# Optimization experiments

Hardware: AMD Instinct MI355X
Metric: run time of the kernel (lower is better)

## Reference

```python
import jax, jax.numpy as jnp
import numpy as np

# Perfect 8-ary tree, 6 levels, level-order node indexing.
K = 8            # children per internal node
D = 512          # embedding_dim
P = 8            # number of dependency types (num_params)
OFF = [0, 1, 9, 73, 585, 4681, 37449]  # level start offsets; N = 37449
N = OFF[-1]


def setup_inputs() -> dict:
    key = jax.random.key(0)
    ks = jax.random.split(key, 8)
    s = 1.0 / np.sqrt(D)  # torch default-ish init scale, avoids LSTM saturation
    return {
        "embeddings": jax.random.normal(ks[0], (N, D), dtype=jnp.float32),
        "dep_types": jax.random.randint(ks[1], (N,), 0, P, dtype=jnp.int32),
        "W_dep": jax.random.normal(ks[2], (P, D, D), dtype=jnp.float32) * s,
        "b_dep": jax.random.normal(ks[3], (P, D), dtype=jnp.float32) * s,
        "W_ih": jax.random.normal(ks[4], (4 * D, D), dtype=jnp.float32) * s,
        "W_hh": jax.random.normal(ks[5], (4 * D, D), dtype=jnp.float32) * s,
        "b_ih": jax.random.normal(ks[6], (4 * D,), dtype=jnp.float32) * s,
        "b_hh": jax.random.normal(ks[7], (4 * D,), dtype=jnp.float32) * s,
    }


def _lstm_final_c(seq, W_ih, W_hh, b_ih, b_hh):
    # seq: [B, T, D]; 1-layer LSTM with zero init state; returns final cell state c_T [B, D]
    B = seq.shape[0]
    h0 = jnp.zeros((B, D), seq.dtype)

    def step(carry, z_t):
        h, c = carry
        gates = z_t @ W_ih.T + h @ W_hh.T + b_ih + b_hh  # [B, 4D]
        i, f, g, o = jnp.split(gates, 4, axis=-1)        # torch gate order i,f,g,o
        i, f, o = jax.nn.sigmoid(i), jax.nn.sigmoid(f), jax.nn.sigmoid(o)
        g = jnp.tanh(g)
        c = f * c + i * g
        h = o * jnp.tanh(c)
        return (h, c), None

    (h, c), _ = jax.lax.scan(step, (h0, h0), jnp.swapaxes(seq, 0, 1))
    return c


def reference(embeddings, dep_types, W_dep, b_dep, W_ih, W_hh, b_ih, b_hh):
    # Leaves (level 5): LSTM over length-1 sequence [x] -> final cell state.
    leaf_x = embeddings[OFF[5]:OFF[6]]                       # [32768, D]
    z = _lstm_final_c(leaf_x[:, None, :], W_ih, W_hh, b_ih, b_hh)

    # Level-synchronous bottom-up sweep (exactly the recursion's per-node math).
    for l in range(4, -1, -1):
        m = OFF[l + 1] - OFF[l]                              # nodes at this level
        child_z = z.reshape(m, K, D)                         # children's subtree codes
        child_dep = dep_types[OFF[l + 1]:OFF[l + 2]].reshape(m, K)
        onehot = jax.nn.one_hot(child_dep, P, dtype=child_z.dtype)  # [m, K, P]
        # per-dep Linear: z_c = W_dep[dep] @ x_c + b_dep[dep]
        zc = jnp.einsum('mkj,pij,mkp->mki', child_z, W_dep, onehot) + onehot @ b_dep
        x = embeddings[OFF[l]:OFF[l + 1]]                    # node's own embedding, last in seq
        seq = jnp.concatenate([zc, x[:, None, :]], axis=1)   # [m, K+1, D]
        z = _lstm_final_c(seq, W_ih, W_hh, b_ih, b_hh)

    return z  # root sentence embedding, [1, D]
```

## Files before the change

### kernel.cpp

```cpp
#include <hip/hip_runtime.h>

typedef __attribute__((ext_vector_type(8))) short short8;
typedef __attribute__((ext_vector_type(4))) float f32x4;
typedef _Float16 half_t;

__device__ __forceinline__ unsigned short f2bf(float x){
  union { float f; unsigned u; } v; v.f = x;
  unsigned r = v.u + 0x7fffu + ((v.u >> 16) & 1u);
  return (unsigned short)(r >> 16);
}
__device__ __forceinline__ float sigm(float x){ return 1.0f / (1.0f + __expf(-x)); }
__device__ __forceinline__ float tanh_(float x){
  float e = __expf(2.0f * x);
  return 1.0f - 2.0f / (e + 1.0f);
}
__device__ __forceinline__ short8 load_bf8_f32(const float* p){
  float4 a = *(const float4*)p;
  float4 b = *(const float4*)(p + 4);
  short8 r;
  r[0]=(short)f2bf(a.x); r[1]=(short)f2bf(a.y); r[2]=(short)f2bf(a.z); r[3]=(short)f2bf(a.w);
  r[4]=(short)f2bf(b.x); r[5]=(short)f2bf(b.y); r[6]=(short)f2bf(b.z); r[7]=(short)f2bf(b.w);
  return r;
}
__device__ __forceinline__ f32x4 mfma16(short8 a, short8 b, f32x4 c){
  return __builtin_amdgcn_mfma_f32_16x16x32_bf16(a, b, c, 0, 0, 0);
}
__device__ __forceinline__ void gload16(const void* g, void* lds){
  __builtin_amdgcn_global_load_lds((const __attribute__((address_space(1))) void*)g,
                                   (__attribute__((address_space(3))) void*)lds, 16, 0, 0);
}
__device__ __forceinline__ f32x4 shfl_xor4(f32x4 v, int m){
  f32x4 r;
  r[0]=__shfl_xor(v[0],m); r[1]=__shfl_xor(v[1],m);
  r[2]=__shfl_xor(v[2],m); r[3]=__shfl_xor(v[3],m);
  return r;
}
__device__ __forceinline__ float pick4(f32x4 v, int k){
  float a = (k&1)? v[1] : v[0];
  float b = (k&1)? v[3] : v[2];
  return (k&2)? b : a;
}
__device__ __forceinline__ f32x4 sel4(f32x4 a0, f32x4 a1, f32x4 a2, f32x4 a3, int k){
  f32x4 x = (k&1)? a1 : a0;
  f32x4 y = (k&1)? a3 : a2;
  return (k&2)? y : x;
}

#define KSTAGE1(AB, BB, off)                                                         \
  {                                                                                  \
    _Pragma("unroll")                                                                \
    for (int q = 0; q < 4; ++q){                                                     \
      gload16(AB[q] + (off), As + (q*32 + w*8)*64);                                  \
      gload16(BB[q] + (off), Bs + (q*32 + w*8)*64);                                  \
    }                                                                                \
  }

#define KCOMP1                                                                       \
  {                                                                                  \
    _Pragma("unroll")                                                                \
    for (int kk = 0; kk < 2; ++kk){                                                  \
      short8 av[4], bv[4];                                                           \
      _Pragma("unroll")                                                              \
      for (int i = 0; i < 4; ++i)                                                    \
        av[i] = *(const short8*)&As[(wm*64 + i*16 + r15)*64 + (((kk*4 + g4) ^ (r15 & 7))*8)]; \
      _Pragma("unroll")                                                              \
      for (int i = 0; i < 4; ++i)                                                    \
        bv[i] = *(const short8*)&Bs[(wn*64 + i*16 + r15)*64 + (((kk*4 + g4) ^ (r15 & 7))*8)]; \
      _Pragma("unroll")                                                              \
      for (int i = 0; i < 4; ++i)                                                    \
        _Pragma("unroll")                                                            \
        for (int j = 0; j < 4; ++j) acc[i][j] = mfma16(av[i], bv[j], acc[i][j]);     \
    }                                                                                \
  }

#define KLOOP1(AB, BB)                                                               \
  for (int kt = 0; kt < 8; ++kt){                                                    \
    KSTAGE1(AB, BB, kt*64)                                                           \
    __syncthreads();                                                                 \
    KCOMP1                                                                           \
    __syncthreads();                                                                 \
  }

#define KSTAGE2(par, AB, BB, off)                                                    \
  {                                                                                  \
    _Pragma("unroll")                                                                \
    for (int q = 0; q < 4; ++q){                                                     \
      gload16(AB[q] + (off), As + (par)*8192 + (q*32 + w*8)*64);                     \
      gload16(BB[q] + (off), Bs + (par)*8192 + (q*32 + w*8)*64);                     \
    }                                                                                \
  }

#define KCOMP2(par)                                                                  \
  {                                                                                  \
    unsigned short* Ac = As + (par)*8192;                                            \
    unsigned short* Bc = Bs + (par)*8192;                                            \
    _Pragma("unroll")                                                                \
    for (int kk = 0; kk < 2; ++kk){                                                  \
      short8 av[4], bv[4];                                                           \
      _Pragma("unroll")                                                              \
      for (int i = 0; i < 4; ++i)                                                    \
        av[i] = *(const short8*)&Ac[(wm*64 + i*16 + r15)*64 + (((kk*4 + g4) ^ (r15 & 7))*8)]; \
      _Pragma("unroll")                                                              \
      for (int i = 0; i < 4; ++i)                                                    \
        bv[i] = *(const short8*)&Bc[(wn*64 + i*16 + r15)*64 + (((kk*4 + g4) ^ (r15 & 7))*8)]; \
      _Pragma("unroll")                                                              \
      for (int i = 0; i < 4; ++i)                                                    \
        _Pragma("unroll")                                                            \
        for (int j = 0; j < 4; ++j) acc[i][j] = mfma16(av[i], bv[j], acc[i][j]);     \
    }                                                                                \
  }

#define KLOOP2(AB, BB)                                                               \
  {                                                                                  \
    KSTAGE2(0, AB, BB, 0)                                                            \
    __syncthreads();                                                                 \
    for (int kt = 0; kt < 8; ++kt){                                                  \
      if (kt < 7){ KSTAGE2((kt+1)&1, AB, BB, (kt+1)*64) }                            \
      KCOMP2(kt&1)                                                                   \
      __syncthreads();                                                               \
    }                                                                                \
  }

__global__ __launch_bounds__(256) void prep_kernel(
    const float* __restrict__ emb, const int* __restrict__ dep,
    const float* __restrict__ W_dep, const float* __restrict__ b_dep,
    const float* __restrict__ W_ih, const float* __restrict__ W_hh,
    const float* __restrict__ b_ih, const float* __restrict__ b_hh,
    unsigned short* __restrict__ embb, unsigned short* __restrict__ Wih_il,
    unsigned short* __restrict__ Whh_il, unsigned short* __restrict__ Wleaf,
    unsigned short* __restrict__ WdT, float* __restrict__ bsum, float* __restrict__ bc,
    int* __restrict__ perm, int* __restrict__ tile_p, int* __restrict__ meta,
    int* __restrict__ perm16, int* __restrict__ tile16, int* __restrict__ meta16)
{
  const int bid = blockIdx.x, tid = threadIdx.x;
  if (bid < 1024){
    for (size_t i = (size_t)bid*256 + tid; i < 2396736ull; i += 1024ull*256)
      *(short8*)(embb + i*8) = load_bf8_f32(emb + i*8);
  } else if (bid < 1536){
    int idx = (bid-1024)*256 + tid; int r = idx >> 6, c8 = idx & 63;
    int sr = (r & 3)*512 + (r >> 2);
    *(short8*)(Wih_il + (size_t)r*512 + c8*8) = load_bf8_f32(W_ih + (size_t)sr*512 + c8*8);
  } else if (bid < 2048){
    int idx = (bid-1536)*256 + tid; int r = idx >> 6, c8 = idx & 63;
    int sr = (r & 3)*512 + (r >> 2);
    *(short8*)(Whh_il + (size_t)r*512 + c8*8) = load_bf8_f32(W_hh + (size_t)sr*512 + c8*8);
  } else if (bid < 2304){
    int idx = (bid-2048)*256 + tid; int r = idx >> 6, c8 = idx & 63;
    int sr = ((r & 1) ? 2 : 0)*512 + (r >> 1);
    *(short8*)(Wleaf + (size_t)r*512 + c8*8) = load_bf8_f32(W_ih + (size_t)sr*512 + c8*8);
  } else if (bid < 2816){
    __shared__ unsigned short tle[64][65];
    int lb = bid - 2304; int p = lb >> 6; int tile = lb & 63;
    int i0 = (tile >> 3)*64, j0 = (tile & 7)*64;
    const float* src = W_dep + (size_t)p*512*512;
    for (int q = 0; q < 16; ++q){
      int e = q*256 + tid; int li = e >> 6, lj = e & 63;
      tle[li][lj] = f2bf(src[(size_t)(i0+li)*512 + (j0+lj)]);
    }
    __syncthreads();
    unsigned short* dst = WdT + (size_t)p*512*512;
    for (int q = 0; q < 16; ++q){
      int e = q*256 + tid; int lj = e >> 6, li = e & 63;
      dst[(size_t)(j0+lj)*512 + (i0+li)] = tle[li][lj];
    }
  } else if (bid < 2824){
    int r = (bid-2816)*256 + tid;
    if (r < 2048){ int g = r & 3, j = r >> 2; bsum[r] = b_ih[g*512+j] + b_hh[g*512+j]; }
  } else if (bid < 2888){
    __shared__ float bd[512];
    int lb = bid - 2824; int p = lb >> 3, ch = lb & 7;
    for (int i = tid; i < 512; i += 256) bd[i] = b_dep[p*512 + i];
    __syncthreads();
    int r = ch*256 + tid; int g = r & 3, j = r >> 2;
    const float* wr = W_ih + (size_t)(g*512 + j)*512;
    float s = 0.0f;
    for (int i = 0; i < 512; ++i) s = fmaf(wr[i], bd[i], s);
    bc[(size_t)p*2048 + r] = s;
  } else if (bid < 2928){
    __shared__ int cnt[8], base[8], fill[8];
    int lb = bid - 2888; const int l = lb >> 3, t = lb & 7;
    const int M_[5]  = {1,8,64,512,4096};
    const int CB_[5] = {1,9,73,585,4681};
    const int MT_[5] = {8,8,8,12,40};
    const int PB_[5] = {69632,61440,53248,40960,0};
    const int TB_[5] = {544,480,416,320,0};
    const int m = M_[l], cb = CB_[l], MT = MT_[l];
    int* pm = perm + PB_[l] + t*MT*128;
    int* tp = tile_p + TB_[l] + t*MT;
    if (tid < 8){ cnt[tid] = 0; fill[tid] = 0; }
    __syncthreads();
    for (int n = tid; n < m; n += 256) atomicAdd(&cnt[dep[cb + n*8 + t]], 1);
    __syncthreads();
    if (tid == 0){
      int tiles = 0;
      for (int p = 0; p < 8; ++p){
        base[p] = tiles*128;
        int g = (cnt[p] + 127) >> 7;
        for (int q = 0; q < g; ++q) tp[tiles + q] = p;
        tiles += g;
      }
      meta[l*8 + t] = tiles;
    }
    __syncthreads();
    for (int i = tid; i < MT*128; i += 256) pm[i] = -1;
    __syncthreads();
    for (int n = tid; n < m; n += 256){
      int p = dep[cb + n*8 + t];
      pm[base[p] + atomicAdd(&fill[p], 1)] = n;
    }
  } else {
    __shared__ int cnt[8], base[8], fill[8];
    int lb = bid - 2928; const int li = lb >> 3, t = lb & 7;
    const int M_[4]  = {512,64,8,1};
    const int CB_[4] = {585,73,9,1};
    const int MT_[4] = {40,8,8,8};
    const int PB_[4] = {0, 5120, 6144, 7168};
    const int TB_[4] = {0, 320, 384, 448};
    const int m = M_[li], cbb = CB_[li], MT = MT_[li];
    int* pm = perm16 + PB_[li] + t*MT*16;
    int* tp = tile16 + TB_[li] + t*MT;
    if (tid < 8){ cnt[tid] = 0; fill[tid] = 0; }
    __syncthreads();
    for (int n = tid; n < m; n += 256) atomicAdd(&cnt[dep[cbb + n*8 + t]], 1);
    __syncthreads();
    if (tid == 0){
      int tiles = 0;
      for (int p = 0; p < 8; ++p){
        base[p] = tiles*16;
        int g = (cnt[p] + 15) >> 4;
        for (int q = 0; q < g; ++q) tp[tiles + q] = p;
        tiles += g;
      }
      meta16[li*8 + t] = tiles;
    }
    __syncthreads();
    for (int i = tid; i < MT*16; i += 256) pm[i] = -1;
    __syncthreads();
    for (int n = tid; n < m; n += 256){
      int p = dep[cbb + n*8 + t];
      pm[base[p] + atomicAdd(&fill[p], 1)] = n;
    }
  }
}

__global__ __launch_bounds__(256) void comboleaf_kernel(
    const unsigned short* __restrict__ Wih_il,
    const unsigned short* __restrict__ WdT,
    unsigned short* __restrict__ Wcombo,
    const unsigned short* __restrict__ embL,
    const unsigned short* __restrict__ Wleaf,
    const float* __restrict__ bsum,
    unsigned short* __restrict__ zo)
{
  __shared__ unsigned short As[8192];
  __shared__ unsigned short Bs[8192];
  const int tid = threadIdx.x, lane = tid & 63, w = tid >> 6;
  const int wm = w >> 1, wn = w & 1;
  const int r15 = lane & 15, g4 = lane >> 4;
  const int kc = ((lane & 7) ^ (lane >> 3)) * 8;

  if (blockIdx.x < 512){
    const int p  = blockIdx.x >> 6;
    const int mt = (blockIdx.x >> 2) & 15;
    const int nb = blockIdx.x & 3;
    const unsigned short* ab[4]; const unsigned short* bb[4];
    #pragma unroll
    for (int q = 0; q < 4; ++q){
      int rl = mt*128 + q*32 + w*8 + (lane >> 3);
      ab[q] = Wih_il + (size_t)rl*512 + kc;
      int br = nb*128 + q*32 + w*8 + (lane >> 3);
      bb[q] = WdT + (size_t)p*262144 + (size_t)br*512 + kc;
    }
    f32x4 acc[4][4] = {};
    KLOOP1(ab, bb)
    unsigned short* Cp = Wcombo + (size_t)p*1048576;
    #pragma unroll
    for (int mi = 0; mi < 4; ++mi)
      #pragma unroll
      for (int ni = 0; ni < 4; ++ni)
        #pragma unroll
        for (int j = 0; j < 4; ++j){
          int row = mt*128 + wm*64 + mi*16 + g4*4 + j;
          int col = nb*128 + wn*64 + ni*16 + r15;
          Cp[(size_t)row*512 + col] = f2bf(acc[mi][ni][j]);
        }
  } else {
    const int lj = blockIdx.x - 512;
    const int mt = (lj & 7)*32 + ((lj >> 3) & 31);
    const int nb = lj >> 8;
    const unsigned short* ab[4]; const unsigned short* bb[4];
    #pragma unroll
    for (int q = 0; q < 4; ++q){
      int rl = mt*128 + q*32 + w*8 + (lane >> 3);
      ab[q] = embL + (size_t)rl*512 + kc;
      int br = nb*128 + q*32 + w*8 + (lane >> 3);
      bb[q] = Wleaf + (size_t)br*512 + kc;
    }
    f32x4 acc[4][4] = {};
    KLOOP1(ab, bb)
    const int g2 = r15 & 1;
    #pragma unroll
    for (int ni = 0; ni < 4; ++ni){
      int ci = nb*128 + wn*64 + ni*16 + r15;
      float b = bsum[4*(ci >> 1) + (g2 ? 2 : 0)];
      #pragma unroll
      for (int mi = 0; mi < 4; ++mi){
        acc[mi][ni][0]+=b; acc[mi][ni][1]+=b; acc[mi][ni][2]+=b; acc[mi][ni][3]+=b;
      }
    }
    #pragma unroll
    for (int mi = 0; mi < 4; ++mi)
      #pragma unroll
      for (int ni = 0; ni < 4; ++ni){
        f32x4 a0 = acc[mi][ni];
        f32x4 a1 = shfl_xor4(a0, 1);
        f32x4 vi_ = g2 ? a1 : a0;
        f32x4 vg_ = g2 ? a0 : a1;
        int jz = (nb*128 + wn*64 + ni*16 + r15) >> 1;
        #pragma unroll
        for (int u = 0; u < 2; ++u){
          int jrow = (g2 << 1) + u;
          float zi = pick4(vi_, jrow), zg = pick4(vg_, jrow);
          int row = mt*128 + wm*64 + mi*16 + g4*4 + jrow;
          zo[(size_t)row*512 + jz] = f2bf(sigm(zi) * tanh_(zg));
        }
      }
  }
}

__device__ __forceinline__ void step_core(
    unsigned short* As, unsigned short* Bs,
    const unsigned short* __restrict__ embb,
    const unsigned short* __restrict__ Wcombo,
    const unsigned short* __restrict__ Wih_il,
    const unsigned short* __restrict__ Whh_il,
    const float* __restrict__ bsum, const float* __restrict__ bc,
    const unsigned short* __restrict__ zin, unsigned short* __restrict__ zo,
    const unsigned short* __restrict__ hi, unsigned short* __restrict__ ho,
    float* __restrict__ cbuf, float* __restrict__ outp,
    const int* __restrict__ pm, const int* __restrict__ tp,
    int node_base, int m, int t, int mt, int nbq, int l)
{
  const int tid = threadIdx.x, lane = tid & 63, w = tid >> 6;
  const int wm = w >> 1, wn = w & 1;
  const int r15 = lane & 15, g4 = lane >> 4;
  const int kc = ((lane & 7) ^ (lane >> 3)) * 8;
  const int first = (t == 0), last = (t == 8);
  const int p = tp ? tp[mt] : 0;

  int nn[4];
  #pragma unroll
  for (int q = 0; q < 4; ++q){
    int rl = mt*128 + q*32 + w*8 + (lane >> 3);
    int n = pm ? pm[rl] : (rl < m ? rl : -1);
    nn[q] = (n < 0) ? 0 : n;
  }
  f32x4 acc[4][4] = {};
  {
    const unsigned short* Bx = (t < 8) ? (Wcombo + (size_t)p*1048576) : Wih_il;
    const unsigned short* ab[4]; const unsigned short* bb[4];
    #pragma unroll
    for (int q = 0; q < 4; ++q){
      ab[q] = (t < 8) ? (zin + ((size_t)nn[q]*8 + t)*512 + kc)
                      : (embb + (size_t)(node_base + nn[q])*512 + kc);
      int br = nbq*128 + q*32 + w*8 + (lane >> 3);
      bb[q] = Bx + (size_t)br*512 + kc;
    }
    KLOOP1(ab, bb)
  }
  if (!first){
    const unsigned short* ab[4]; const unsigned short* bb[4];
    #pragma unroll
    for (int q = 0; q < 4; ++q){
      ab[q] = hi + (size_t)nn[q]*512 + kc;
      int br = nbq*128 + q*32 + w*8 + (lane >> 3);
      bb[q] = Whh_il + (size_t)br*512 + kc;
    }
    KLOOP1(ab, bb)
  }
  const int gate = r15 & 3;
  #pragma unroll
  for (int ni = 0; ni < 4; ++ni){
    int ci = nbq*128 + wn*64 + ni*16 + r15;
    float b = bsum[ci] + ((t < 8) ? bc[(size_t)p*2048 + ci] : 0.0f);
    #pragma unroll
    for (int mi = 0; mi < 4; ++mi){
      acc[mi][ni][0]+=b; acc[mi][ni][1]+=b; acc[mi][ni][2]+=b; acc[mi][ni][3]+=b;
    }
  }
  const int jr = r15 & 3;
  #pragma unroll
  for (int mi = 0; mi < 4; ++mi){
    int rl = mt*128 + wm*64 + mi*16 + g4*4 + jr;
    int n = pm ? pm[rl] : (rl < m ? rl : -1);
    #pragma unroll
    for (int ni = 0; ni < 4; ++ni){
      f32x4 a0 = acc[mi][ni];
      f32x4 a1 = shfl_xor4(a0, 1);
      f32x4 a2 = shfl_xor4(a0, 2);
      f32x4 a3 = shfl_xor4(a1, 2);
      f32x4 vi_ = sel4(a0,a1,a2,a3, gate);
      f32x4 vf_ = sel4(a0,a1,a2,a3, gate^1);
      f32x4 vg_ = sel4(a0,a1,a2,a3, gate^2);
      f32x4 vo_ = sel4(a0,a1,a2,a3, gate^3);
      float xi = pick4(vi_, jr), xf = pick4(vf_, jr);
      float xg = pick4(vg_, jr), xo = pick4(vo_, jr);
      if (n >= 0){
        int jz = nbq*32 + wn*16 + ni*4 + (r15 >> 2);
        size_t idx = (size_t)n*512 + jz;
        float i_ = sigm(xi), f_ = sigm(xf), g_ = tanh_(xg), o_ = sigm(xo);
        float cold = first ? 0.0f : cbuf[idx];
        float cn = fmaf(f_, cold, i_*g_);
        if (!last){ cbuf[idx] = cn; ho[idx] = f2bf(o_*tanh_(cn)); }
        else { if (l > 0) zo[idx] = f2bf(cn); else outp[idx] = cn; }
      }
    }
  }
}

__global__ __launch_bounds__(256) void step_kernel(
    const unsigned short* __restrict__ embb,
    const unsigned short* __restrict__ Wcombo,
    const unsigned short* __restrict__ Wih_il,
    const unsigned short* __restrict__ Whh_il,
    const float* __restrict__ bsum, const float* __restrict__ bc,
    const unsigned short* __restrict__ zin, unsigned short* __restrict__ zo,
    const unsigned short* __restrict__ hi, unsigned short* __restrict__ ho,
    float* __restrict__ cbuf, float* __restrict__ outp,
    const int* __restrict__ perm_t, const int* __restrict__ tile_t,
    const int* __restrict__ meta_t,
    int fixed_nt, int MTcap, int node_base, int m, int t, int l)
{
  __shared__ unsigned short As[8192];
  __shared__ unsigned short Bs[8192];
  int ntiles = meta_t ? *meta_t : fixed_nt;
  if (ntiles > MTcap) ntiles = MTcap;
  const int njobs = ntiles * 16;
  const int chunk = (njobs + 7) >> 3;
  const int g = blockIdx.x & 7, i = blockIdx.x >> 3;
  const int job = g*chunk + i;
  if (i >= chunk || job >= njobs) return;
  const int mt = job % ntiles, nbq = job / ntiles;
  step_core(As, Bs, embb, Wcombo, Wih_il, Whh_il, bsum, bc, zin, zo, hi, ho,
            cbuf, outp, perm_t, tile_t, node_base, m, t, mt, nbq, l);
}

__global__ __launch_bounds__(256) void gatex16(
    const unsigned short* __restrict__ embb,
    const unsigned short* __restrict__ Wcombo,
    const unsigned short* __restrict__ Wih_il,
    const float* __restrict__ bsum, const float* __restrict__ bc,
    const unsigned short* __restrict__ zin,
    half_t* __restrict__ gx, unsigned short* __restrict__ h0out,
    float* __restrict__ cbuf,
    const int* __restrict__ perm16l, const int* __restrict__ tile16l,
    const int* __restrict__ meta16l,
    int MT, int m, int node_base)
{
  __shared__ unsigned short As[2048];
  __shared__ unsigned short Bs[16384];
  const int jt = blockIdx.x >> 4, cb = blockIdx.x & 15;
  int t, mt, p = 0;
  const int* pm = nullptr;
  if (jt < 8*MT){
    t = jt / MT; mt = jt - t*MT;
    if (mt >= meta16l[t]) return;
    pm = perm16l + t*MT*16;
    p = tile16l[t*MT + mt];
  } else {
    t = 8; mt = jt - 8*MT;
  }
  const int tid = threadIdx.x, lane = tid & 63, w = tid >> 6;
  const int r15 = lane & 15, g4 = lane >> 4;
  const int kc = ((lane & 7) ^ (lane >> 3)) * 8;

  const unsigned short* aptr = nullptr;
  if (w < 2){
    int lr = w*8 + (lane >> 3);
    int n;
    if (t < 8) n = pm[mt*16 + lr];
    else { int r = mt*16 + lr; n = (r < m) ? r : -1; }
    if (n < 0) n = 0;
    const unsigned short* base = (t < 8) ? (zin + ((size_t)n*8 + t)*512)
                                         : (embb + (size_t)(node_base + n)*512);
    aptr = base + (((lane & 7) ^ (lr & 7)) * 8);
  }
  const unsigned short* BxP = (t < 8) ? (Wcombo + (size_t)p*1048576) : Wih_il;
  const unsigned short* bb[4];
  #pragma unroll
  for (int q = 0; q < 4; ++q)
    bb[q] = BxP + (size_t)(cb*128 + q*32 + w*8 + (lane >> 3))*512 + kc;

  f32x4 acc[2] = {};
  if (w < 2) gload16(aptr, As + w*512);
  #pragma unroll
  for (int q = 0; q < 4; ++q) gload16(bb[q], Bs + (q*32 + w*8)*64);
  __syncthreads();
  for (int kt = 0; kt < 8; ++kt){
    if (kt < 7){
      const int pn = (kt + 1) & 1;
      if (w < 2) gload16(aptr + (kt+1)*64, As + pn*1024 + w*512);
      #pragma unroll
      for (int q = 0; q < 4; ++q)
        gload16(bb[q] + (kt+1)*64, Bs + pn*8192 + (q*32 + w*8)*64);
    }
    const int pc = kt & 1;
    #pragma unroll
    for (int kk = 0; kk < 2; ++kk){
      short8 a = *(const short8*)&As[pc*1024 + r15*64 + (((kk*4 + g4) ^ (r15 & 7))*8)];
      #pragma unroll
      for (int ni = 0; ni < 2; ++ni){
        short8 b = *(const short8*)&Bs[pc*8192 + (w*32 + ni*16 + r15)*64 + (((kk*4 + g4) ^ (r15 & 7))*8)];
        acc[ni] = mfma16(a, b, acc[ni]);
      }
    }
    __syncthreads();
  }

  #pragma unroll
  for (int ni = 0; ni < 2; ++ni){
    int ci = cb*128 + w*32 + ni*16 + r15;
    float b = bsum[ci] + ((t < 8) ? bc[(size_t)p*2048 + ci] : 0.0f);
    acc[ni][0]+=b; acc[ni][1]+=b; acc[ni][2]+=b; acc[ni][3]+=b;
  }

  if (t == 0){
    const int gate = r15 & 3;
    const int jr = r15 & 3;
    const int lr = g4*4 + jr;
    const int n = pm[mt*16 + lr];
    #pragma unroll
    for (int ni = 0; ni < 2; ++ni){
      f32x4 a0 = acc[ni];
      f32x4 a1 = shfl_xor4(a0, 1);
      f32x4 a2 = shfl_xor4(a0, 2);
      f32x4 a3 = shfl_xor4(a1, 2);
      f32x4 vi_ = sel4(a0,a1,a2,a3, gate);
      f32x4 vg_ = sel4(a0,a1,a2,a3, gate^2);
      f32x4 vo_ = sel4(a0,a1,a2,a3, gate^3);
      float xi = pick4(vi_, jr);
      float xg = pick4(vg_, jr);
      float xo = pick4(vo_, jr);
      if (n >= 0){
        int jz = cb*32 + w*8 + ni*4 + (r15 >> 2);
        size_t idx = (size_t)n*512 + jz;
        float cn = sigm(xi) * tanh_(xg);
        cbuf[idx] = cn;
        h0out[idx] = f2bf(sigm(xo) * tanh_(cn));
      }
    }
  } else {
    #pragma unroll
    for (int ni = 0; ni < 2; ++ni){
      int ci = cb*128 + w*32 + ni*16 + r15;
      #pragma unroll
      for (int j = 0; j < 4; ++j){
        int lr = g4*4 + j;
        int n = (t < 8) ? pm[mt*16 + lr]
                        : ((mt*16 + lr < m) ? mt*16 + lr : -1);
        if (n >= 0) gx[((size_t)t*m + n)*2048 + ci] = (half_t)acc[ni][j];
      }
    }
  }
}

__global__ __launch_bounds__(256) void hstep_kernel(
    const unsigned short* __restrict__ Whh_il,
    const half_t* __restrict__ gx,
    const unsigned short* __restrict__ hi, unsigned short* __restrict__ ho,
    float* __restrict__ cbuf,
    unsigned short* __restrict__ zo, float* __restrict__ outp,
    int m, int t, int last)
{
  __shared__ unsigned short As[16384];
  __shared__ unsigned short Bs[16384];
  const int mt = blockIdx.x >> 4, nbq = blockIdx.x & 15;
  const int tid = threadIdx.x, lane = tid & 63, w = tid >> 6;
  const int wm = w >> 1, wn = w & 1;
  const int r15 = lane & 15, g4 = lane >> 4;
  const int kc = ((lane & 7) ^ (lane >> 3)) * 8;

  int nn[4];
  #pragma unroll
  for (int q = 0; q < 4; ++q){
    int rl = mt*128 + q*32 + w*8 + (lane >> 3);
    nn[q] = (rl < m) ? rl : 0;
  }
  const unsigned short* ab[4]; const unsigned short* bb[4];
  #pragma unroll
  for (int q = 0; q < 4; ++q){
    ab[q] = hi + (size_t)nn[q]*512 + kc;
    int br = nbq*128 + q*32 + w*8 + (lane >> 3);
    bb[q] = Whh_il + (size_t)br*512 + kc;
  }
  f32x4 acc[4][4] = {};
  KLOOP2(ab, bb)

  #pragma unroll
  for (int mi = 0; mi < 4; ++mi)
    #pragma unroll
    for (int ni = 0; ni < 4; ++ni){
      int ci = nbq*128 + wn*64 + ni*16 + r15;
      #pragma unroll
      for (int j = 0; j < 4; ++j){
        int rl = mt*128 + wm*64 + mi*16 + g4*4 + j;
        if (rl < m) acc[mi][ni][j] += (float)gx[((size_t)t*m + rl)*2048 + ci];
      }
    }

  const int gate = r15 & 3;
  const int jr = r15 & 3;
  #pragma unroll
  for (int mi = 0; mi < 4; ++mi){
    int rl = mt*128 + wm*64 + mi*16 + g4*4 + jr;
    int n = (rl < m) ? rl : -1;
    #pragma unroll
    for (int ni = 0; ni < 4; ++ni){
      f32x4 a0 = acc[mi][ni];
      f32x4 a1 = shfl_xor4(a0, 1);
      f32x4 a2 = shfl_xor4(a0, 2);
      f32x4 a3 = shfl_xor4(a1, 2);
      f32x4 vi_ = sel4(a0,a1,a2,a3, gate);
      f32x4 vf_ = sel4(a0,a1,a2,a3, gate^1);
      f32x4 vg_ = sel4(a0,a1,a2,a3, gate^2);
      f32x4 vo_ = sel4(a0,a1,a2,a3, gate^3);
      float xi = pick4(vi_, jr), xf = pick4(vf_, jr);
      float xg = pick4(vg_, jr), xo = pick4(vo_, jr);
      if (n >= 0){
        int jz = nbq*32 + wn*16 + ni*4 + (r15 >> 2);
        size_t idx = (size_t)n*512 + jz;
        float i_ = sigm(xi), f_ = sigm(xf), g_ = tanh_(xg), o_ = sigm(xo);
        float cn = fmaf(f_, cbuf[idx], i_*g_);
        if (!last){ cbuf[idx] = cn; ho[idx] = f2bf(o_*tanh_(cn)); }
        else { if (zo) zo[idx] = f2bf(cn); else outp[idx] = cn; }
      }
    }
  }
}

extern "C" void kernel_launch(void* const* d_in, const int* in_sizes, int n_in,
                              void* d_out, int out_size, void* d_ws, size_t ws_size,
                              hipStream_t stream)
{
  (void)in_sizes; (void)n_in; (void)out_size; (void)ws_size;
  const float* emb   = (const float*)d_in[0];
  const int*   dep   = (const int*)  d_in[1];
  const float* W_dep = (const float*)d_in[2];
  const float* b_dep = (const float*)d_in[3];
  const float* W_ih  = (const float*)d_in[4];
  const float* W_hh  = (const float*)d_in[5];
  const float* b_ih  = (const float*)d_in[6];
  const float* b_hh  = (const float*)d_in[7];
  float* out = (float*)d_out;

  unsigned short* embb   = (unsigned short*)d_ws;
  unsigned short* Wih_il = embb   + 19173888ull;
  unsigned short* Whh_il = Wih_il + 1048576ull;
  unsigned short* Wleaf  = Whh_il + 1048576ull;
  unsigned short* WdT    = Wleaf  + 524288ull;
  unsigned short* Wcombo = WdT    + 2097152ull;
  unsigned short* Z0     = Wcombo + 8388608ull;
  unsigned short* Z1     = Z0     + 16777216ull;
  unsigned short* hA     = Z1     + 2097152ull;
  unsigned short* hB     = hA     + 2097152ull;
  float* cbuf  = (float*)(hB + 2097152ull);
  float* bsum  = cbuf + 2097152ull;
  float* bc    = bsum + 2048;
  int*  perm   = (int*)(bc + 16384);
  int*  tile_p = perm + 77824;
  int*  meta   = tile_p + 608;
  int*  perm16 = meta + 40;
  int*  tile16 = perm16 + 8192;
  int*  meta16 = tile16 + 512;
  half_t* gx   = (half_t*)(meta16 + 32);

  prep_kernel<<<2960, 256, 0, stream>>>(emb, dep, W_dep, b_dep, W_ih, W_hh, b_ih, b_hh,
                                        embb, Wih_il, Whh_il, Wleaf, WdT, bsum, bc,
                                        perm, tile_p, meta, perm16, tile16, meta16);
  comboleaf_kernel<<<2560, 256, 0, stream>>>(Wih_il, WdT, Wcombo,
                                             embb + (size_t)4681*512, Wleaf, bsum, Z0);

  for (int t = 0; t <= 8; ++t){
    const unsigned short* hi = (t & 1) ? hA : hB;
    unsigned short* ho       = (t & 1) ? hB : hA;
    int grid = (t < 8) ? 40*16 : 32*16;
    step_kernel<<<grid, 256, 0, stream>>>(
        embb, Wcombo, Wih_il, Whh_il, bsum, bc,
        Z0, Z1, hi, ho, cbuf, nullptr,
        (t < 8) ? (perm + t*40*128) : nullptr,
        (t < 8) ? (tile_p + t*40) : nullptr,
        (t < 8) ? (meta + 4*8 + t) : nullptr,
        32, 40, 585, 4096, t, 4);
  }

  struct LvG { int m, node_base, p16, t16, m16, MT, nt8, mtiles; };
  const LvG LG[4] = {
    {512, 73, 0,    0,   0,  40, 32, 4},
    {64,  9,  5120, 320, 8,  8,  4,  1},
    {8,   1,  6144, 384, 16, 8,  1,  1},
    {1,   0,  7168, 448, 24, 8,  1,  1}};
  for (int k = 0; k < 4; ++k){
    const int l = 3 - k;
    const unsigned short* zin = (l & 1) ? Z1 : Z0;
    unsigned short* zo        = (l & 1) ? Z0 : Z1;
    gatex16<<<(8*LG[k].MT + LG[k].nt8)*16, 256, 0, stream>>>(
        embb, Wcombo, Wih_il, bsum, bc, zin, gx, hA, cbuf,
        perm16 + LG[k].p16, tile16 + LG[k].t16, meta16 + LG[k].m16,
        LG[k].MT, LG[k].m, LG[k].node_base);
    for (int t = 1; t <= 8; ++t){
      const unsigned short* hi = (t & 1) ? hA : hB;
      unsigned short* ho       = (t & 1) ? hB : hA;
      hstep_kernel<<<LG[k].mtiles*16, 256, 0, stream>>>(
          Whh_il, gx, hi, ho, cbuf,
          (t == 8 && l > 0) ? zo : nullptr, (l == 0) ? out : nullptr,
          LG[k].m, t, (t == 8));
    }
  }
}
```

Measured before the change: 1.285 ms.

## Hoist level-4 input-gate GEMMs into one batched kernel before the recurrence

For the 4096-node level, all nine timesteps' input projections (child codes through the combined dep/W_ih weights, plus the node embedding) are computed in one wide gatex128 launch and stored as fp16 gate pre-activations. Each recurrent step then runs only the h·W_hh GEMM via hstep_kernel. Previously every step_kernel recomputed both GEMMs serially. This takes the input GEMM off the sequential critical path and raises parallelism, at the cost of a large fp16 workspace buffer and extra memory traffic. The old path is kept as a fallback when the workspace is too small.

Measured after the change: 1.441 ms. 12.1% more time.

```diff
diff --git a/kernel.cpp b/kernel.cpp
--- a/kernel.cpp
+++ b/kernel.cpp
@@ -445,6 +445,109 @@
             cbuf, outp, perm_t, tile_t, node_base, m, t, mt, nbq, l);
 }
 
+__global__ __launch_bounds__(256) void gatex128(
+    const unsigned short* __restrict__ embb,
+    const unsigned short* __restrict__ Wcombo,
+    const unsigned short* __restrict__ Wih_il,
+    const float* __restrict__ bsum, const float* __restrict__ bc,
+    const unsigned short* __restrict__ zin,
+    half_t* __restrict__ gx, unsigned short* __restrict__ h0out,
+    float* __restrict__ cbuf,
+    const int* __restrict__ perm_l, const int* __restrict__ tile_l,
+    const int* __restrict__ meta_l,
+    int MT, int m, int node_base)
+{
+  __shared__ unsigned short As[8192];
+  __shared__ unsigned short Bs[8192];
+  const int jt = blockIdx.x >> 4, nbq = blockIdx.x & 15;
+  int t, mt, p = 0;
+  const int* pm = nullptr;
+  if (jt < 8*MT){
+    t = jt / MT; mt = jt - t*MT;
+    if (mt >= meta_l[t]) return;
+    pm = perm_l + t*MT*128;
+    p = tile_l[t*MT + mt];
+  } else {
+    t = 8; mt = jt - 8*MT;
+  }
+  const int tid = threadIdx.x, lane = tid & 63, w = tid >> 6;
+  const int wm = w >> 1, wn = w & 1;
+  const int r15 = lane & 15, g4 = lane >> 4;
+  const int kc = ((lane & 7) ^ (lane >> 3)) * 8;
+
+  int nn[4];
+  #pragma unroll
+  for (int q = 0; q < 4; ++q){
+    int rl = mt*128 + q*32 + w*8 + (lane >> 3);
+    int n = pm ? pm[rl] : (rl < m ? rl : -1);
+    nn[q] = (n < 0) ? 0 : n;
+  }
+  const unsigned short* Bx = (t < 8) ? (Wcombo + (size_t)p*1048576) : Wih_il;
+  const unsigned short* ab[4]; const unsigned short* bb[4];
+  #pragma unroll
+  for (int q = 0; q < 4; ++q){
+    ab[q] = (t < 8) ? (zin + ((size_t)nn[q]*8 + t)*512 + kc)
+                    : (embb + (size_t)(node_base + nn[q])*512 + kc);
+    int br = nbq*128 + q*32 + w*8 + (lane >> 3);
+    bb[q] = Bx + (size_t)br*512 + kc;
+  }
+  f32x4 acc[4][4] = {};
+  KLOOP1(ab, bb)
+
+  #pragma unroll
+  for (int ni = 0; ni < 4; ++ni){
+    int ci = nbq*128 + wn*64 + ni*16 + r15;
+    float b = bsum[ci] + ((t < 8) ? bc[(size_t)p*2048 + ci] : 0.0f);
+    #pragma unroll
+    for (int mi = 0; mi < 4; ++mi){
+      acc[mi][ni][0]+=b; acc[mi][ni][1]+=b; acc[mi][ni][2]+=b; acc[mi][ni][3]+=b;
+    }
+  }
+
+  if (t == 0){
+    const int gate = r15 & 3;
+    const int jr = r15 & 3;
+    #pragma unroll
+    for (int mi = 0; mi < 4; ++mi){
+      int rl = mt*128 + wm*64 + mi*16 + g4*4 + jr;
+      int n = pm ? pm[rl] : (rl < m ? rl : -1);
+      #pragma unroll
+      for (int ni = 0; ni < 4; ++ni){
+        f32x4 a0 = acc[mi][ni];
+        f32x4 a1 = shfl_xor4(a0, 1);
+        f32x4 a2 = shfl_xor4(a0, 2);
+        f32x4 a3 = shfl_xor4(a1, 2);
+        f32x4 vi_ = sel4(a0,a1,a2,a3, gate);
+        f32x4 vg_ = sel4(a0,a1,a2,a3, gate^2);
+        f32x4 vo_ = sel4(a0,a1,a2,a3, gate^3);
+        float xi = pick4(vi_, jr);
+        float xg = pick4(vg_, jr);
+        float xo = pick4(vo_, jr);
+        if (n >= 0){
+          int jz = nbq*32 + wn*16 + ni*4 + (r15 >> 2);
+          size_t idx = (size_t)n*512 + jz;
+          float cn = sigm(xi) * tanh_(xg);
+          cbuf[idx] = cn;
+          h0out[idx] = f2bf(sigm(xo) * tanh_(cn));
+        }
+      }
+    }
+  } else {
+    #pragma unroll
+    for (int mi = 0; mi < 4; ++mi)
+      #pragma unroll
+      for (int ni = 0; ni < 4; ++ni){
+        int ci = nbq*128 + wn*64 + ni*16 + r15;
+        #pragma unroll
+        for (int j = 0; j < 4; ++j){
+          int rl = mt*128 + wm*64 + mi*16 + g4*4 + j;
+          int n = pm ? pm[rl] : (rl < m ? rl : -1);
+          if (n >= 0) gx[((size_t)t*m + n)*2048 + ci] = (half_t)acc[mi][ni][j];
+        }
+      }
+  }
+}
+
 __global__ __launch_bounds__(256) void gatex16(
     const unsigned short* __restrict__ embb,
     const unsigned short* __restrict__ Wcombo,
@@ -642,7 +745,7 @@
                               void* d_out, int out_size, void* d_ws, size_t ws_size,
                               hipStream_t stream)
 {
-  (void)in_sizes; (void)n_in; (void)out_size; (void)ws_size;
+  (void)in_sizes; (void)n_in; (void)out_size;
   const float* emb   = (const float*)d_in[0];
   const int*   dep   = (const int*)  d_in[1];
   const float* W_dep = (const float*)d_in[2];
@@ -673,6 +776,9 @@
   int*  tile16 = perm16 + 8192;
   int*  meta16 = tile16 + 512;
   half_t* gx   = (half_t*)(meta16 + 32);
+  half_t* gx4  = gx + 9437184ull;
+  const size_t need4 = (size_t)((char*)(gx4 + 75497472ull) - (char*)d_ws);
+  const int use_split4 = (ws_size >= need4);
 
   prep_kernel<<<2960, 256, 0, stream>>>(emb, dep, W_dep, b_dep, W_ih, W_hh, b_ih, b_hh,
                                         embb, Wih_il, Whh_il, Wleaf, WdT, bsum, bc,
@@ -680,17 +786,30 @@
   comboleaf_kernel<<<2560, 256, 0, stream>>>(Wih_il, WdT, Wcombo,
                                              embb + (size_t)4681*512, Wleaf, bsum, Z0);
 
-  for (int t = 0; t <= 8; ++t){
-    const unsigned short* hi = (t & 1) ? hA : hB;
-    unsigned short* ho       = (t & 1) ? hB : hA;
-    int grid = (t < 8) ? 40*16 : 32*16;
-    step_kernel<<<grid, 256, 0, stream>>>(
-        embb, Wcombo, Wih_il, Whh_il, bsum, bc,
-        Z0, Z1, hi, ho, cbuf, nullptr,
-        (t < 8) ? (perm + t*40*128) : nullptr,
-        (t < 8) ? (tile_p + t*40) : nullptr,
-        (t < 8) ? (meta + 4*8 + t) : nullptr,
-        32, 40, 585, 4096, t, 4);
+  if (use_split4){
+    gatex128<<<(8*40 + 32)*16, 256, 0, stream>>>(
+        embb, Wcombo, Wih_il, bsum, bc, Z0, gx4, hA, cbuf,
+        perm, tile_p, meta + 4*8, 40, 4096, 585);
+    for (int t = 1; t <= 8; ++t){
+      const unsigned short* hi = (t & 1) ? hA : hB;
+      unsigned short* ho       = (t & 1) ? hB : hA;
+      hstep_kernel<<<32*16, 256, 0, stream>>>(
+          Whh_il, gx4, hi, ho, cbuf,
+          (t == 8) ? Z1 : nullptr, nullptr, 4096, t, (t == 8));
+    }
+  } else {
+    for (int t = 0; t <= 8; ++t){
+      const unsigned short* hi = (t & 1) ? hA : hB;
+      unsigned short* ho       = (t & 1) ? hB : hA;
+      int grid = (t < 8) ? 40*16 : 32*16;
+      step_kernel<<<grid, 256, 0, stream>>>(
+          embb, Wcombo, Wih_il, Whh_il, bsum, bc,
+          Z0, Z1, hi, ho, cbuf, nullptr,
+          (t < 8) ? (perm + t*40*128) : nullptr,
+          (t < 8) ? (tile_p + t*40) : nullptr,
+          (t < 8) ? (meta + 4*8 + t) : nullptr,
+          32, 40, 585, 4096, t, 4);
+    }
   }
 
   struct LvG { int m, node_base, p16, t16, m16, MT, nt8, mtiles; };
```
